# Performance work log

Hardware: AMD Instinct MI355X
Metric: run time of the kernel (lower is better)

The kernel has to match this reference:

```python
import jax, jax.numpy as jnp
import numpy as np

N = 512      # nodes
F_IN = 16    # raw node features; adjacency channels = 2*F_IN = 32
H = 64       # hidden
HF = 64      # hidden_final
C = 10       # num_classes
L = 3        # num_layers
E = 16384    # edges (avg degree 32)
EPS = 1e-5


def setup_inputs() -> dict:
    key = jax.random.key(0)
    ks = iter(jax.random.split(key, 40))
    rn = lambda shape, s=0.05: jax.random.normal(next(ks), shape, jnp.float32) * s
    inp = {
        'x': jax.random.normal(next(ks), (N, F_IN), jnp.float32),
        'edge_index': jax.random.randint(next(ks), (2, E), 0, N),
        # no_prop FeatureExtractor
        'np1_w': rn((HF, 2 * F_IN)), 'np1_b': rn((HF,)),
        'np2_w': rn((HF, 2 * F_IN)), 'np3_w': rn((HF, HF)),
        # first PowerfulLayer (in = 2*F_IN)
        'c0_m1_w': rn((H, 2 * F_IN)), 'c0_m1_b': rn((H,)),
        'c0_m2_w': rn((H, 2 * F_IN)), 'c0_m2_b': rn((H,)),
        'c0_m4_w': rn((H, 2 * F_IN + H)), 'c0_m4_b': rn((H,)),
        # remaining L-1 PowerfulLayers (stacked)
        'cm1_w': rn((L - 1, H, H)), 'cm1_b': rn((L - 1, H)),
        'cm2_w': rn((L - 1, H, H)), 'cm2_b': rn((L - 1, H)),
        'cm4_w': rn((L - 1, H, 2 * H)), 'cm4_b': rn((L - 1, H)),
        # batchnorms (training-mode stats; affine params)
        'bn_g': jnp.ones((L, H), jnp.float32), 'bn_b': jnp.zeros((L, H), jnp.float32),
        # per-layer FeatureExtractors (stacked)
        'fe1_w': rn((L, HF, H)), 'fe1_b': rn((L, HF)),
        'fe2_w': rn((L, HF, H)), 'fe3_w': rn((L, HF, HF)),
        # after_conv and final linear
        'ac_w': rn((HF, HF)), 'ac_b': rn((HF,)),
        'fl_w': rn((C, HF)), 'fl_b': rn((C,)),
    }
    return inp


def _lin(x, w, b=None):
    y = x @ w.T
    return y if b is None else y + b


def _extractor(u, w1, b1, w2, w3):
    # u: [B, N, N, F]; graph_class=True, aggr='add'
    n = u.shape[1]
    trace = jnp.einsum('biif->bf', u)                     # sum of diagonal entries
    out1 = _lin(trace / n, w1, b1)
    s = (u.sum(axis=(1, 2)) - trace) / (n * (n - 1))      # off-diagonal mean-ish
    out = out1 + _lin(s, w2)
    return out + _lin(jax.nn.relu(out), w3)


def _powerful(u, m1w, m1b, m2w, m2b, m4w, m4b):
    # UnitMLP with 1 layer == 1x1 conv == per-position linear (no ReLU)
    o1 = jnp.einsum('bijc,oc->bijo', u, m1w) + m1b        # [B,N,N,H]
    o2 = jnp.einsum('bijc,oc->bijo', u, m2w) + m2b
    mult = jnp.einsum('bikh,bkjh->bijh', o1, o2)          # per-channel NxN matmul
    return _lin(jnp.concatenate([mult, u], axis=-1), m4w, m4b)


def _batchnorm(u, g, b):
    # BatchNorm2d in training mode: stats over (batch, N, N) per channel, biased var
    mean = u.mean(axis=(0, 1, 2))
    var = u.var(axis=(0, 1, 2))
    return (u - mean) * jax.lax.rsqrt(var + EPS) * g + b


def reference(x, edge_index, np1_w, np1_b, np2_w, np3_w,
              c0_m1_w, c0_m1_b, c0_m2_w, c0_m2_b, c0_m4_w, c0_m4_b,
              cm1_w, cm1_b, cm2_w, cm2_b, cm4_w, cm4_b,
              bn_g, bn_b, fe1_w, fe1_b, fe2_w, fe3_w,
              ac_w, ac_b, fl_w, fl_b):
    n = x.shape[0]
    src, dst = edge_index[0], edge_index[1]
    edge_attr = jnp.concatenate([x[src], x[dst]], axis=-1)          # [E, 2F]
    A = jnp.zeros((n, n, edge_attr.shape[-1]), x.dtype).at[src, dst].add(edge_attr)
    u = A[None]                                                      # [1,N,N,2F]

    out = _extractor(u, np1_w, np1_b, np2_w, np3_w)
    nlayers = bn_g.shape[0]
    for l in range(nlayers):
        if l == 0:
            u = _powerful(u, c0_m1_w, c0_m1_b, c0_m2_w, c0_m2_b, c0_m4_w, c0_m4_b)
        else:
            u = _powerful(u, cm1_w[l - 1], cm1_b[l - 1], cm2_w[l - 1], cm2_b[l - 1],
                          cm4_w[l - 1], cm4_b[l - 1])
        u = _batchnorm(u, bn_g[l], bn_b[l])
        out = out + _extractor(u, fe1_w[l], fe1_b[l], fe2_w[l], fe3_w[l])

    out = jax.nn.relu(out) / nlayers
    out = out + jax.nn.relu(_lin(out, ac_w, ac_b))   # layer_after_conv
    # dropout with p=0.0 / eval mode is identity
    out = _lin(out, fl_w, fl_b)
    return jax.nn.log_softmax(out, axis=-1)          # [1, num_classes]
```

## Files before the change

### kernel.cpp

```cpp
#include <hip/hip_runtime.h>
#include <hip/hip_bf16.h>

#define Nn   512
#define NN   262144
#define EDG  16384

typedef unsigned short u16;
typedef unsigned int u32;
typedef short v8s __attribute__((ext_vector_type(8)));
typedef float v4f __attribute__((ext_vector_type(4)));
typedef u16 u16x8 __attribute__((ext_vector_type(8)));

__device__ __forceinline__ float b2f(u16 u) {
    union { unsigned int i; float f; } v; v.i = ((unsigned int)u) << 16; return v.f;
}
__device__ __forceinline__ u16 f2b(float f) {
    union { float f; unsigned int i; } v; v.f = f;
    unsigned int r = (v.i + 0x7FFFu + ((v.i >> 16) & 1u)) >> 16;
    return (u16)r;
}

__global__ void sentinel_kernel(float* __restrict__ out, float val) {
    if (threadIdx.x < 10) out[threadIdx.x] = val;
}

__global__ void cvt_weights(const float* __restrict__ s0, const float* __restrict__ s1,
                            const float* __restrict__ s2, const float* __restrict__ s3,
                            const float* __restrict__ s4, const float* __restrict__ s5,
                            u16* __restrict__ dst) {
    int t = blockIdx.x * 256 + threadIdx.x;
    if (t >= 43008) return;
    float v;
    if      (t < 2048)  v = s0[t];
    else if (t < 4096)  v = s1[t - 2048];
    else if (t < 10240) v = s2[t - 4096];
    else if (t < 18432) v = s3[t - 10240];
    else if (t < 26624) v = s4[t - 18432];
    else                v = s5[t - 26624];
    dst[t] = f2b(v);
}

__global__ void scatter_edges(const float* __restrict__ x, const int* __restrict__ ei,
                              float* __restrict__ A) {
    int t = blockIdx.x * 256 + threadIdx.x;
    if (t >= EDG * 32) return;
    int e = t >> 5, c = t & 31;
    int s = ei[e], d = ei[EDG + e];
    float v = (c < 16) ? x[s * 16 + c] : x[d * 16 + (c - 16)];
    atomicAdd(A + ((size_t)s * Nn + d) * 32 + c, v);
}

__global__ __launch_bounds__(256) void finalize_u0(const float* __restrict__ A,
                                                   u16* __restrict__ u0,
                                                   float* __restrict__ total) {
    __shared__ u16 L[32 * 258];
    __shared__ float red[4][32];
    int t = threadIdx.x;
    int p0 = blockIdx.x * 256;
    const float* Ar = A + (size_t)(p0 + t) * 32;
    float v[32];
#pragma unroll
    for (int c = 0; c < 32; ++c) v[c] = Ar[c];
#pragma unroll
    for (int c = 0; c < 32; ++c) L[c * 258 + t] = f2b(v[c]);
    int wv = t >> 6;
#pragma unroll
    for (int c = 0; c < 32; ++c) {
        float r = v[c];
        for (int off = 32; off > 0; off >>= 1) r += __shfl_down(r, off);
        if ((t & 63) == 0) red[wv][c] = r;
    }
    __syncthreads();
    if (t < 32) atomicAdd(total + t, red[0][t] + red[1][t] + red[2][t] + red[3][t]);
    int off = (t & 31) * 8, rb = t >> 5;
#pragma unroll
    for (int pass = 0; pass < 4; ++pass) {
        int c = pass * 8 + rb;
        u16x8 w = *(const u16x8*)(L + c * 258 + off);
        *(u16x8*)(u0 + (size_t)c * NN + p0 + off) = w;
    }
}

__global__ void trace_raw_cm(const u16* __restrict__ ucm, float* __restrict__ trraw) {
    int c = blockIdx.x, t = threadIdx.x;
    const u16* base = ucm + (size_t)c * NN;
    float s = b2f(base[(size_t)(2 * t) * 513]) + b2f(base[(size_t)(2 * t + 1) * 513]);
    for (int off = 32; off > 0; off >>= 1) s += __shfl_down(s, off);
    __shared__ float r[4];
    if ((t & 63) == 0) r[t >> 6] = s;
    __syncthreads();
    if (t == 0) trraw[c] = r[0] + r[1] + r[2] + r[3];
}

template<int NCH>
__global__ __launch_bounds__(256) void conv12_t(
    const u16* __restrict__ src,
    const float* __restrict__ sc, const float* __restrict__ sh,
    const u16* __restrict__ w1, const float* __restrict__ b1,
    const u16* __restrict__ w2, const float* __restrict__ b2,
    u16* __restrict__ dst1, u16* __restrict__ dst2)
{
    __shared__ u16 LS[8320];
    const int C = NCH * 32;
    const int t = threadIdx.x;
    const int P0 = blockIdx.x * 128;
    const int lane = t & 63, wave = t >> 6;
    const int l15 = lane & 15, quad = lane >> 4;
    const int pw = wave * 32;
    const int sr = t >> 4;
    const int so = (t & 15) * 8;

    u16x8 pf[NCH][2];
#pragma unroll
    for (int kc = 0; kc < NCH; ++kc)
#pragma unroll
        for (int ps = 0; ps < 2; ++ps)
            pf[kc][ps] = *(const u16x8*)(src + (size_t)(kc * 32 + ps * 16 + sr) * NN + P0 + so);

    v4f acc[2][4][2];
#pragma unroll
    for (int s = 0; s < 2; ++s)
#pragma unroll
        for (int mt = 0; mt < 4; ++mt)
#pragma unroll
            for (int nt = 0; nt < 2; ++nt) acc[s][mt][nt] = (v4f){0.f, 0.f, 0.f, 0.f};

    {
        u16* Ln = LS;
#pragma unroll
        for (int ps = 0; ps < 2; ++ps) {
            int c = ps * 16 + sr;
            u16x8 v = pf[0][ps];
            if (sc) {
                float s = sc[c], f = sh[c];
#pragma unroll
                for (int j = 0; j < 8; ++j) v[j] = f2b(b2f(v[j]) * s + f);
            }
            *(u16x8*)(Ln + c * 130 + so) = v;
        }
    }
    __syncthreads();
#pragma unroll
    for (int kc = 0; kc < NCH; ++kc) {
        if (kc + 1 < NCH) {
            u16* Ln = LS + ((kc + 1) & 1) * 4160;
#pragma unroll
            for (int ps = 0; ps < 2; ++ps) {
                int c = ps * 16 + sr;
                int cg = (kc + 1) * 32 + c;
                u16x8 v = pf[kc + 1][ps];
                if (sc) {
                    float s = sc[cg], f = sh[cg];
#pragma unroll
                    for (int j = 0; j < 8; ++j) v[j] = f2b(b2f(v[j]) * s + f);
                }
                *(u16x8*)(Ln + c * 130 + so) = v;
            }
        }
        v8s af1[4], af2[4];
#pragma unroll
        for (int mt = 0; mt < 4; ++mt) {
            af1[mt] = *(const v8s*)(w1 + (mt * 16 + l15) * C + kc * 32 + quad * 8);
            af2[mt] = *(const v8s*)(w2 + (mt * 16 + l15) * C + kc * 32 + quad * 8);
        }
        const u16* Lb = LS + (kc & 1) * 4160;
#pragma unroll
        for (int nt = 0; nt < 2; ++nt) {
            const int p = pw + nt * 16 + l15;
            v8s b;
#pragma unroll
            for (int j = 0; j < 8; ++j) b[j] = (short)Lb[(quad * 8 + j) * 130 + p];
#pragma unroll
            for (int mt = 0; mt < 4; ++mt) {
                acc[0][mt][nt] = __builtin_amdgcn_mfma_f32_16x16x32_bf16(af1[mt], b, acc[0][mt][nt], 0, 0, 0);
                acc[1][mt][nt] = __builtin_amdgcn_mfma_f32_16x16x32_bf16(af2[mt], b, acc[1][mt][nt], 0, 0, 0);
            }
        }
        if (kc + 1 < NCH) __syncthreads();
    }
#pragma unroll
    for (int s = 0; s < 2; ++s) {
        __syncthreads();
        const float* bb = s ? b2 : b1;
#pragma unroll
        for (int mt = 0; mt < 4; ++mt)
#pragma unroll
            for (int r = 0; r < 4; ++r) {
                const int h = mt * 16 + quad * 4 + r;
                const float bv = bb[h];
#pragma unroll
                for (int nt = 0; nt < 2; ++nt)
                    LS[h * 130 + pw + nt * 16 + l15] = f2b(acc[s][mt][nt][r] + bv);
            }
        __syncthreads();
        u16* dd = s ? dst2 : dst1;
#pragma unroll
        for (int ps = 0; ps < 4; ++ps) {
            int h = ps * 16 + sr;
            u16x8 v = *(const u16x8*)(LS + h * 130 + so);
            __builtin_nontemporal_store(v, (u16x8*)(dd + (size_t)h * NN + P0 + so));
        }
    }
}

template<int NCH>
__global__ __launch_bounds__(256) void conv4_t(
    const u16* __restrict__ mult, const u16* __restrict__ u,
    const float* __restrict__ sc, const float* __restrict__ sh,
    const u16* __restrict__ w, const float* __restrict__ bias,
    u16* __restrict__ dst,
    float* __restrict__ psum, float* __restrict__ psq, float* __restrict__ ptr)
{
    __shared__ u16 LS[8320];
    __shared__ float R1[64][4], R2[64][4];
    const int K = NCH * 32;
    const int t = threadIdx.x;
    const int P0 = blockIdx.x * 128;
    const int lane = t & 63, wave = t >> 6;
    const int l15 = lane & 15, quad = lane >> 4;
    const int pw = wave * 32;
    const int sr = t >> 4;
    const int so = (t & 15) * 8;

    u16x8 pf[NCH][2];
#pragma unroll
    for (int kc = 0; kc < NCH; ++kc)
#pragma unroll
        for (int ps = 0; ps < 2; ++ps) {
            int cg = kc * 32 + ps * 16 + sr;
            const u16* gp = (cg < 64) ? (mult + (size_t)cg * NN + P0 + so)
                                      : (u + (size_t)(cg - 64) * NN + P0 + so);
            pf[kc][ps] = *(const u16x8*)gp;
        }

    v4f acc[4][2];
#pragma unroll
    for (int mt = 0; mt < 4; ++mt)
#pragma unroll
        for (int nt = 0; nt < 2; ++nt) acc[mt][nt] = (v4f){0.f, 0.f, 0.f, 0.f};

#pragma unroll
    for (int ps = 0; ps < 2; ++ps)
        *(u16x8*)(LS + (ps * 16 + sr) * 130 + so) = pf[0][ps];
    __syncthreads();
#pragma unroll
    for (int kc = 0; kc < NCH; ++kc) {
        if (kc + 1 < NCH) {
            u16* Ln = LS + ((kc + 1) & 1) * 4160;
#pragma unroll
            for (int ps = 0; ps < 2; ++ps) {
                int c = ps * 16 + sr;
                int cg = (kc + 1) * 32 + c;
                u16x8 v = pf[kc + 1][ps];
                if (cg >= 64 && sc) {
                    float s = sc[cg - 64], f = sh[cg - 64];
#pragma unroll
                    for (int j = 0; j < 8; ++j) v[j] = f2b(b2f(v[j]) * s + f);
                }
                *(u16x8*)(Ln + c * 130 + so) = v;
            }
        }
        v8s af[4];
#pragma unroll
        for (int mt = 0; mt < 4; ++mt)
            af[mt] = *(const v8s*)(w + (mt * 16 + l15) * K + kc * 32 + quad * 8);
        const u16* Lb = LS + (kc & 1) * 4160;
#pragma unroll
        for (int nt = 0; nt < 2; ++nt) {
            const int p = pw + nt * 16 + l15;
            v8s b;
#pragma unroll
            for (int j = 0; j < 8; ++j) b[j] = (short)Lb[(quad * 8 + j) * 130 + p];
#pragma unroll
            for (int mt = 0; mt < 4; ++mt)
                acc[mt][nt] = __builtin_amdgcn_mfma_f32_16x16x32_bf16(af[mt], b, acc[mt][nt], 0, 0, 0);
        }
        if (kc + 1 < NCH) __syncthreads();
    }
    __syncthreads();
#pragma unroll
    for (int mt = 0; mt < 4; ++mt)
#pragma unroll
        for (int r = 0; r < 4; ++r) {
            const int h = mt * 16 + quad * 4 + r;
            const float bv = bias[h];
#pragma unroll
            for (int nt = 0; nt < 2; ++nt)
                LS[h * 130 + pw + nt * 16 + l15] = f2b(acc[mt][nt][r] + bv);
        }
    __syncthreads();
    {
        int c = t >> 2, q = t & 3;
        const u16* row = LS + c * 130 + q * 32;
        float s = 0.f, s2 = 0.f;
#pragma unroll
        for (int i = 0; i < 32; ++i) { float v = b2f(row[i]); s += v; s2 += v * v; }
        R1[c][q] = s; R2[c][q] = s2;
    }
    __syncthreads();
    {
        int i = P0 >> 9, j0 = P0 & 511;
        int blk = blockIdx.x;
        if (t < 64) {
            psum[t * 2048 + blk] = R1[t][0] + R1[t][1] + R1[t][2] + R1[t][3];
            psq[t * 2048 + blk]  = R2[t][0] + R2[t][1] + R2[t][2] + R2[t][3];
            if (j0 <= i && i < j0 + 128) ptr[t * 512 + i] = b2f(LS[t * 130 + (i - j0)]);
        }
    }
#pragma unroll
    for (int ps = 0; ps < 4; ++ps) {
        int h = ps * 16 + sr;
        u16x8 v = *(const u16x8*)(LS + h * 130 + so);
        __builtin_nontemporal_store(v, (u16x8*)(dst + (size_t)h * NN + P0 + so));
    }
}

__global__ __launch_bounds__(512, 2) void bmm_mfma256(const u16* __restrict__ Aall,
                                                      const u16* __restrict__ Ball,
                                                      u16* __restrict__ Call) {
    __shared__ u16 LA[2][16384];
    __shared__ u16 LB[2][16384];

    const int bid = blockIdx.x;
    const int h  = ((bid >> 5) << 3) | (bid & 7);
    const int qq = (bid >> 3) & 3;
    const int ty = qq >> 1, tx = qq & 1;
    const int t = threadIdx.x;
    const int l = t & 63, w = t >> 6;
    const int l15 = l & 15, quad = l >> 4;
    const int wr = w >> 2, wc = w & 3;

    const u16* Ap = Aall + (size_t)h * NN + (size_t)ty * 256 * 512;
    const u16* Bp = Ball + (size_t)h * NN + tx * 256;
    u16* Cp = Call + (size_t)h * NN;

    const int a_m = l >> 3;
    const int a_kg = (l & 7) ^ a_m;
    const u16* ApL = Ap + (size_t)a_m * 512 + a_kg * 8;

    v4f acc[8][4];
#pragma unroll
    for (int mt = 0; mt < 8; ++mt)
#pragma unroll
        for (int nt = 0; nt < 4; ++nt) acc[mt][nt] = (v4f){0.f, 0.f, 0.f, 0.f};

    uint2 eB[4], oB[4];

#define BMM_BLOAD(K0)                                                         \
    _Pragma("unroll")                                                         \
    for (int L = 0; L < 4; ++L) {                                             \
        const int p = w + 8 * L;                                              \
        const u16* s_ = Bp + (size_t)((K0) + 2 * p) * 512 + l * 4;            \
        eB[L] = *(const uint2*)s_;                                            \
        oB[L] = *(const uint2*)(s_ + 512);                                    \
    }

#define BMM_ALOAD(BUF, K0)                                                    \
    _Pragma("unroll")                                                         \
    for (int c = 0; c < 4; ++c) {                                             \
        const int cc = w * 4 + c;                                             \
        __builtin_amdgcn_global_load_lds(                                     \
            (const void*)(ApL + (size_t)cc * 4096 + (K0)),                    \
            (void*)&LA[BUF][cc * 512], 16, 0, 0);                             \
    }

#define BMM_BWRITE(BUF)                                                       \
    {                                                                         \
        char* base_ = (char*)&LB[BUF][0];                                     \
        _Pragma("unroll")                                                     \
        for (int L = 0; L < 4; ++L) {                                         \
            const int p = w + 8 * L;                                          \
            const int gk = p >> 2, wd = p & 3;                                \
            u32 e0 = eB[L].x, e1 = eB[L].y, o0 = oB[L].x, o1 = oB[L].y;       \
            u32 pk0 = (e0 & 0xFFFFu) | (o0 << 16);                            \
            u32 pk1 = (e0 >> 16) | (o0 & 0xFFFF0000u);                        \
            u32 pk2 = (e1 & 0xFFFFu) | (o1 << 16);                            \
            u32 pk3 = (e1 >> 16) | (o1 & 0xFFFF0000u);                        \
            _Pragma("unroll")                                                 \
            for (int q = 0; q < 4; ++q) {                                     \
                const int j = l * 4 + q;                                      \
                const int g = gk ^ (j & 7) ^ ((j >> 3) & 7);                  \
                u32 v_ = (q == 0) ? pk0 : (q == 1) ? pk1 : (q == 2) ? pk2 : pk3; \
                *(u32*)(base_ + j * 128 + (g << 4) + wd * 4) = v_;            \
            }                                                                 \
        }                                                                     \
    }

#define BMM_COMPUTE(BUF)                                                      \
    _Pragma("unroll")                                                         \
    for (int kk = 0; kk < 2; ++kk) {                                          \
        v8s af_[8], bf_[4];                                                   \
        const char* baseA_ = (const char*)&LA[BUF][0];                        \
        const char* baseB_ = (const char*)&LB[BUF][0];                        \
        _Pragma("unroll")                                                     \
        for (int mt = 0; mt < 8; ++mt) {                                      \
            const int m = wr * 128 + mt * 16 + l15;                           \
            const int g = (kk * 4 + quad) ^ (m & 7);                          \
            af_[mt] = *(const v8s*)(baseA_ + m * 128 + (g << 4));             \
        }                                                                     \
        _Pragma("unroll")                                                     \
        for (int nt = 0; nt < 4; ++nt) {                                      \
            const int j = wc * 64 + nt * 16 + l15;                            \
            const int g = (kk * 4 + quad) ^ (j & 7) ^ ((j >> 3) & 7);         \
            bf_[nt] = *(const v8s*)(baseB_ + j * 128 + (g << 4));             \
        }                                                                     \
        _Pragma("unroll")                                                     \
        for (int mt = 0; mt < 8; ++mt)                                        \
            _Pragma("unroll")                                                 \
            for (int nt = 0; nt < 4; ++nt)                                    \
                acc[mt][nt] = __builtin_amdgcn_mfma_f32_16x16x32_bf16(        \
                    af_[mt], bf_[nt], acc[mt][nt], 0, 0, 0);                  \
    }

    BMM_BLOAD(0)
    BMM_ALOAD(0, 0)
    BMM_BWRITE(0)
    __syncthreads();

#pragma unroll 2
    for (int ts = 0; ts < 8; ++ts) {
        const int cur = ts & 1;
        if (ts < 7) {
            BMM_BLOAD((ts + 1) * 64)
            BMM_ALOAD(cur ^ 1, (ts + 1) * 64)
        }
        BMM_COMPUTE(cur)
        if (ts < 7) {
            BMM_BWRITE(cur ^ 1)
            __syncthreads();
        }
    }

#pragma unroll
    for (int mt = 0; mt < 8; ++mt)
#pragma unroll
        for (int r = 0; r < 4; ++r) {
            const int i = ty * 256 + wr * 128 + mt * 16 + quad * 4 + r;
#pragma unroll
            for (int nt = 0; nt < 4; ++nt) {
                const int j = tx * 256 + wc * 64 + nt * 16 + l15;
                Cp[(size_t)i * 512 + j] = f2b(acc[mt][nt][r]);
            }
        }
#undef BMM_BLOAD
#undef BMM_ALOAD
#undef BMM_BWRITE
#undef BMM_COMPUTE
}

__global__ __launch_bounds__(256) void bn_finalize(
    const float* __restrict__ psum, const float* __restrict__ psq,
    const float* __restrict__ ptr,
    const float* __restrict__ g, const float* __restrict__ b,
    float* __restrict__ scale, float* __restrict__ shift,
    float* __restrict__ ttl) {
    int c = blockIdx.x, t = threadIdx.x;
    float s = 0.f, q = 0.f, tr = 0.f;
    for (int k = t; k < 2048; k += 256) { s += psum[c * 2048 + k]; q += psq[c * 2048 + k]; }
    for (int k = t; k < 512; k += 256) tr += ptr[c * 512 + k];
    for (int off = 32; off > 0; off >>= 1) {
        s += __shfl_down(s, off); q += __shfl_down(q, off); tr += __shfl_down(tr, off);
    }
    __shared__ float r1[4], r2[4], r3[4];
    if ((t & 63) == 0) { r1[t >> 6] = s; r2[t >> 6] = q; r3[t >> 6] = tr; }
    __syncthreads();
    if (t == 0) {
        s = r1[0] + r1[1] + r1[2] + r1[3];
        q = r2[0] + r2[1] + r2[2] + r2[3];
        tr = r3[0] + r3[1] + r3[2] + r3[3];
        float mean = s * (1.f / 262144.f);
        float var = q * (1.f / 262144.f) - mean * mean;
        float sc = g[c] * rsqrtf(fmaxf(var, 0.f) + 1e-5f);
        float sh = b[c] - mean * sc;
        scale[c] = sc;
        shift[c] = sh;
        ttl[64 + c] = sc * s + 262144.f * sh;
        ttl[c]      = sc * tr + 512.f * sh;
    }
}

__global__ __launch_bounds__(256) void extractor_par(
    const float* __restrict__ tt,
    const float* __restrict__ np1w, const float* __restrict__ np1b,
    const float* __restrict__ np2w, const float* __restrict__ np3w,
    const float* __restrict__ fe1w, const float* __restrict__ fe1b,
    const float* __restrict__ fe2w, const float* __restrict__ fe3w,
    float* __restrict__ oacc_part) {
    __shared__ float red[64][4];
    __shared__ float xo[64];
    const int li = blockIdx.x;
    const int t = threadIdx.x;
    const int h = t >> 2, q = t & 3;
    const int C = (li == 0) ? 32 : 64;
    const float* w1 = (li == 0) ? np1w : fe1w + (li - 1) * 4096;
    const float* b1 = (li == 0) ? np1b : fe1b + (li - 1) * 64;
    const float* w2 = (li == 0) ? np2w : fe2w + (li - 1) * 4096;
    const float* w3 = (li == 0) ? np3w : fe3w + (li - 1) * 4096;
    const float* tr = tt + li * 128;
    const float* to = tr + 64;
    const int cpq = C >> 2;
    float p = 0.f;
    for (int i = 0; i < cpq; ++i) {
        int c = q * cpq + i;
        p += (tr[c] * (1.f / 512.f)) * w1[h * C + c]
           + ((to[c] - tr[c]) * (1.f / (512.f * 511.f))) * w2[h * C + c];
    }
    red[h][q] = p;
    __syncthreads();
    if (q == 0) xo[h] = b1[h] + red[h][0] + red[h][1] + red[h][2] + red[h][3];
    __syncthreads();
    float o = xo[h];
    float p3 = 0.f;
    for (int i = 0; i < 16; ++i) {
        int f = q * 16 + i;
        p3 += fmaxf(xo[f], 0.f) * w3[h * 64 + f];
    }
    __syncthreads();
    red[h][q] = p3;
    __syncthreads();
    if (q == 0) oacc_part[li * 64 + h] = o + red[h][0] + red[h][1] + red[h][2] + red[h][3];
}

__global__ __launch_bounds__(256) void head_par(
    const float* __restrict__ oacc_part,
    const float* __restrict__ acw, const float* __restrict__ acb,
    const float* __restrict__ flw, const float* __restrict__ flb,
    float* __restrict__ out) {
    __shared__ float x[64], x2[64], red[64][4], l[10];
    const int t = threadIdx.x;
    const int h = t >> 2, q = t & 3;
    if (q == 0) {
        float oa = oacc_part[h] + oacc_part[64 + h] + oacc_part[128 + h] + oacc_part[192 + h];
        x[h] = fmaxf(oa, 0.f) * (1.f / 3.f);
    }
    __syncthreads();
    float p = 0.f;
    for (int i = 0; i < 16; ++i) { int f = q * 16 + i; p += x[f] * acw[h * 64 + f]; }
    red[h][q] = p;
    __syncthreads();
    if (q == 0) {
        float y = acb[h] + red[h][0] + red[h][1] + red[h][2] + red[h][3];
        x2[h] = x[h] + fmaxf(y, 0.f);
    }
    __syncthreads();
    if (t < 40) {
        int hh = t >> 2, qq = t & 3;
        float p2 = 0.f;
        for (int i = 0; i < 16; ++i) { int f = qq * 16 + i; p2 += x2[f] * flw[hh * 64 + f]; }
        red[hh][qq] = p2;
    }
    __syncthreads();
    if (t < 10) l[t] = flb[t] + red[t][0] + red[t][1] + red[t][2] + red[t][3];
    __syncthreads();
    if (t == 0) {
        float m = l[0];
        for (int i = 1; i < 10; ++i) m = fmaxf(m, l[i]);
        float se = 0.f;
        for (int i = 0; i < 10; ++i) se += expf(l[i] - m);
        float ls = m + logf(se);
        for (int i = 0; i < 10; ++i) out[i] = l[i] - ls;
    }
}

extern "C" void kernel_launch(void* const* d_in, const int* in_sizes, int n_in,
                              void* d_out, int out_size, void* d_ws, size_t ws_size,
                              hipStream_t stream) {
    float* out = (float*)d_out;

    static const int exp_sizes[28] = {
        8192, 32768,
        2048, 64, 2048, 4096,
        2048, 64, 2048, 64, 6144, 64,
        8192, 128, 8192, 128, 16384, 128,
        192, 192,
        12288, 192, 12288, 12288,
        4096, 64, 640, 10
    };
    bool ok = (n_in == 28);
    if (ok) for (int i = 0; i < 28; ++i) if (in_sizes[i] != exp_sizes[i]) ok = false;
    if (!ok) { sentinel_kernel<<<1, 64, 0, stream>>>(out, -5.0f); return; }

    const size_t RSZ = (size_t)NN * 64 * 2;
    const size_t BIG_OFF = 8192 + 90112;
    if (ws_size < BIG_OFF + 4 * RSZ) {
        sentinel_kernel<<<1, 64, 0, stream>>>(out, -7.0f);
        return;
    }

    const float* x     = (const float*)d_in[0];
    const int*   ei    = (const int*)d_in[1];
    const float* np1w  = (const float*)d_in[2];
    const float* np1b  = (const float*)d_in[3];
    const float* np2w  = (const float*)d_in[4];
    const float* np3w  = (const float*)d_in[5];
    const float* c0m1b = (const float*)d_in[7];
    const float* c0m2b = (const float*)d_in[9];
    const float* c0m4b = (const float*)d_in[11];
    const float* cm1b  = (const float*)d_in[13];
    const float* cm2b  = (const float*)d_in[15];
    const float* cm4b  = (const float*)d_in[17];
    const float* bng   = (const float*)d_in[18];
    const float* bnb   = (const float*)d_in[19];
    const float* fe1w  = (const float*)d_in[20];
    const float* fe1b  = (const float*)d_in[21];
    const float* fe2w  = (const float*)d_in[22];
    const float* fe3w  = (const float*)d_in[23];
    const float* acw   = (const float*)d_in[24];
    const float* acb   = (const float*)d_in[25];
    const float* flw   = (const float*)d_in[26];
    const float* flb   = (const float*)d_in[27];

    char* ws = (char*)d_ws;
    float* small = (float*)ws;
    float* tt    = small;
    float* scl   = small + 512;
    float* shf   = small + 576;
    float* oaccp = small + 640;

    u16* arena = (u16*)(ws + 8192);

    char* big = ws + BIG_OFF;
    u16* S0 = (u16*)(big + 0 * RSZ);
    u16* S1 = (u16*)(big + 1 * RSZ);
    u16* S2 = (u16*)(big + 2 * RSZ);
    u16* S3 = (u16*)(big + 3 * RSZ);
    float* Abuf = (float*)S2;

    float* psum = (float*)S2;
    float* psq  = psum + 64 * 2048;
    float* ptr  = psq + 64 * 2048;

    hipMemsetAsync(small, 0, 4096, stream);
    hipMemsetAsync(Abuf, 0, (size_t)NN * 32 * 4, stream);

    cvt_weights<<<168, 256, 0, stream>>>((const float*)d_in[6], (const float*)d_in[8],
                                         (const float*)d_in[10], (const float*)d_in[12],
                                         (const float*)d_in[14], (const float*)d_in[16], arena);
    scatter_edges<<<2048, 256, 0, stream>>>(x, ei, Abuf);
    finalize_u0<<<1024, 256, 0, stream>>>(Abuf, S0, tt + 64);
    trace_raw_cm<<<32, 256, 0, stream>>>(S0, tt);

    u16* U[3]  = { S0, S1, S0 };
    u16* O1[3] = { S1, S0, S1 };
    u16* R[3]  = { S1, S0, S1 };

    const float *aff_s = nullptr, *aff_h = nullptr;

    for (int l = 0; l < 3; ++l) {
        int Cin = (l == 0) ? 32 : 64;
        const u16 *w1b, *w2b, *w4b;
        const float *b1, *b2, *b4;
        if (l == 0) {
            w1b = arena;            b1 = c0m1b;
            w2b = arena + 2048;     b2 = c0m2b;
            w4b = arena + 4096;     b4 = c0m4b;
        } else {
            int m = l - 1;
            w1b = arena + 10240 + m * 4096;  b1 = cm1b + m * 64;
            w2b = arena + 18432 + m * 4096;  b2 = cm2b + m * 64;
            w4b = arena + 26624 + m * 8192;  b4 = cm4b + m * 64;
        }
        if (Cin == 32)
            conv12_t<1><<<2048, 256, 0, stream>>>(U[l], aff_s, aff_h, w1b, b1, w2b, b2, O1[l], S2);
        else
            conv12_t<2><<<2048, 256, 0, stream>>>(U[l], aff_s, aff_h, w1b, b1, w2b, b2, O1[l], S2);
        bmm_mfma256<<<256, 512, 0, stream>>>(O1[l], S2, S3);
        if (Cin == 32)
            conv4_t<3><<<2048, 256, 0, stream>>>(S3, U[l], aff_s, aff_h, w4b, b4, R[l], psum, psq, ptr);
        else
            conv4_t<4><<<2048, 256, 0, stream>>>(S3, U[l], aff_s, aff_h, w4b, b4, R[l], psum, psq, ptr);
        bn_finalize<<<64, 256, 0, stream>>>(psum, psq, ptr, bng + l * 64, bnb + l * 64,
                                            scl, shf, tt + (l + 1) * 128);
        aff_s = scl; aff_h = shf;
    }
    extractor_par<<<4, 256, 0, stream>>>(tt, np1w, np1b, np2w, np3w,
                                         fe1w, fe1b, fe2w, fe3w, oaccp);
    head_par<<<1, 256, 0, stream>>>(oaccp, acw, acb, flw, flb, out);
}
```

Measured before the change: 467.1 us.

## Restructure conv12 into persistent 512-thread blocks with swizzled position-major LDS tiles

Replaces the conv12 kernel with a version where each 512-thread block handles 512 positions over four 128-position tiles. Weights and biases are loaded into registers once per block, global loads for the next tile are double-buffered against MFMA compute, and the LDS tile is stored position-major with an XOR swizzle so B fragments can be read as 16-byte vectors instead of eight scalar reads. The aim is to cut redundant weight loads, LDS bank conflicts and per-block overhead. In exchange, outputs are now written as scattered 2-byte nontemporal stores instead of coalesced 16-byte stores, and register pressure rises.

```diff
diff --git a/kernel.cpp b/kernel.cpp
--- a/kernel.cpp
+++ b/kernel.cpp
@@ -18,6 +18,11 @@
     union { float f; unsigned int i; } v; v.f = f;
     unsigned int r = (v.i + 0x7FFFu + ((v.i >> 16) & 1u)) >> 16;
     return (u16)r;
+}
+__device__ __forceinline__ u32 aff2(u32 x, float s, float h) {
+    float lo = b2f((u16)(x & 0xFFFFu)) * s + h;
+    float hi = b2f((u16)(x >> 16)) * s + h;
+    return (u32)f2b(lo) | ((u32)f2b(hi) << 16);
 }
 
 __global__ void sentinel_kernel(float* __restrict__ out, float val) {
@@ -92,115 +97,153 @@
     if (t == 0) trraw[c] = r[0] + r[1] + r[2] + r[3];
 }
 
-template<int NCH>
-__global__ __launch_bounds__(256) void conv12_t(
+template<int CIN>
+__global__ __launch_bounds__(512, 4) void conv12_s(
     const u16* __restrict__ src,
     const float* __restrict__ sc, const float* __restrict__ sh,
     const u16* __restrict__ w1, const float* __restrict__ b1,
     const u16* __restrict__ w2, const float* __restrict__ b2,
     u16* __restrict__ dst1, u16* __restrict__ dst2)
 {
-    __shared__ u16 LS[8320];
-    const int C = NCH * 32;
+    constexpr int G    = CIN / 8;
+    constexpr int LOGG = (CIN == 64) ? 3 : 2;
+    constexpr int ROWB = CIN * 2;
+    constexpr int KC   = CIN / 32;
+    constexpr int PASSES = CIN / 32;
+
+    __shared__ char LB[2][128 * ROWB];
+
     const int t = threadIdx.x;
-    const int P0 = blockIdx.x * 128;
-    const int lane = t & 63, wave = t >> 6;
+    const int lane = t & 63, w = t >> 6;
     const int l15 = lane & 15, quad = lane >> 4;
-    const int pw = wave * 32;
-    const int sr = t >> 4;
-    const int so = (t & 15) * 8;
-
-    u16x8 pf[NCH][2];
-#pragma unroll
-    for (int kc = 0; kc < NCH; ++kc)
-#pragma unroll
-        for (int ps = 0; ps < 2; ++ps)
-            pf[kc][ps] = *(const u16x8*)(src + (size_t)(kc * 32 + ps * 16 + sr) * NN + P0 + so);
-
-    v4f acc[2][4][2];
-#pragma unroll
-    for (int s = 0; s < 2; ++s)
-#pragma unroll
-        for (int mt = 0; mt < 4; ++mt)
-#pragma unroll
-            for (int nt = 0; nt < 2; ++nt) acc[s][mt][nt] = (v4f){0.f, 0.f, 0.f, 0.f};
-
-    {
-        u16* Ln = LS;
-#pragma unroll
-        for (int ps = 0; ps < 2; ++ps) {
-            int c = ps * 16 + sr;
-            u16x8 v = pf[0][ps];
-            if (sc) {
-                float s = sc[c], f = sh[c];
-#pragma unroll
-                for (int j = 0; j < 8; ++j) v[j] = f2b(b2f(v[j]) * s + f);
+    const int wr = w >> 1;
+    const int wn = w & 1;
+    const size_t Pblk = (size_t)blockIdx.x * 512;
+
+    const int cpair = (CIN == 64) ? (t >> 4) : (t >> 5);
+    const int pg    = (CIN == 64) ? (t & 15) : (t & 31);
+    const int g0    = cpair >> 2;
+    const int word  = cpair & 3;
+    const u16* srcA = src + (size_t)(2 * cpair) * NN;
+    float s0 = 1.f, h0 = 0.f, s1 = 1.f, h1 = 0.f;
+    const bool aff = (sc != nullptr);
+    if (aff) { s0 = sc[2 * cpair]; h0 = sh[2 * cpair]; s1 = sc[2 * cpair + 1]; h1 = sh[2 * cpair + 1]; }
+
+    v8s af[2][KC];
+#pragma unroll
+    for (int mt = 0; mt < 2; ++mt) {
+        const int row = wr * 32 + mt * 16 + l15;
+        const u16* Wm = (row < 64) ? (w1 + row * CIN) : (w2 + (row - 64) * CIN);
+#pragma unroll
+        for (int kc = 0; kc < KC; ++kc)
+            af[mt][kc] = *(const v8s*)(Wm + kc * 32 + quad * 8);
+    }
+    float bias[2][4];
+#pragma unroll
+    for (int mt = 0; mt < 2; ++mt)
+#pragma unroll
+        for (int r = 0; r < 4; ++r) {
+            const int row = wr * 32 + mt * 16 + quad * 4 + r;
+            bias[mt][r] = (row < 64) ? b1[row] : b2[row - 64];
+        }
+
+    v4f acc[2][4];
+#pragma unroll
+    for (int mt = 0; mt < 2; ++mt)
+#pragma unroll
+        for (int nt = 0; nt < 4; ++nt) acc[mt][nt] = (v4f){0.f, 0.f, 0.f, 0.f};
+
+    uint2 ea[PASSES], eb[PASSES];
+
+#define C12_LOAD(T)                                                           \
+    _Pragma("unroll")                                                         \
+    for (int pp = 0; pp < PASSES; ++pp) {                                     \
+        const int p0_ = (pg + ((CIN == 64) ? 16 : 0) * pp) * 4;               \
+        const u16* sp_ = srcA + Pblk + (size_t)(T) * 128 + p0_;               \
+        ea[pp] = *(const uint2*)sp_;                                          \
+        eb[pp] = *(const uint2*)(sp_ + NN);                                   \
+    }
+
+#define C12_WRITE(BUF)                                                        \
+    {                                                                         \
+        char* Lb_ = LB[BUF];                                                  \
+        _Pragma("unroll")                                                     \
+        for (int pp = 0; pp < PASSES; ++pp) {                                 \
+            const int p0_ = (pg + ((CIN == 64) ? 16 : 0) * pp) * 4;           \
+            u32 A0 = ea[pp].x, A1 = ea[pp].y, B0 = eb[pp].x, B1 = eb[pp].y;   \
+            if (aff) {                                                        \
+                A0 = aff2(A0, s0, h0); A1 = aff2(A1, s0, h0);                 \
+                B0 = aff2(B0, s1, h1); B1 = aff2(B1, s1, h1);                 \
+            }                                                                 \
+            u32 pk0 = (A0 & 0xFFFFu) | (B0 << 16);                            \
+            u32 pk1 = (A0 >> 16) | (B0 & 0xFFFF0000u);                        \
+            u32 pk2 = (A1 & 0xFFFFu) | (B1 << 16);                            \
+            u32 pk3 = (A1 >> 16) | (B1 & 0xFFFF0000u);                        \
+            _Pragma("unroll")                                                 \
+            for (int w4 = 0; w4 < 4; ++w4) {                                  \
+                const int p_ = p0_ + w4;                                      \
+                const int g_ = g0 ^ (p_ & (G - 1)) ^ ((p_ >> LOGG) & (G - 1));\
+                u32 v_ = (w4 == 0) ? pk0 : (w4 == 1) ? pk1 : (w4 == 2) ? pk2 : pk3; \
+                *(u32*)(Lb_ + p_ * ROWB + g_ * 16 + word * 4) = v_;           \
+            }                                                                 \
+        }                                                                     \
+    }
+
+#define C12_COMPUTE(BUF)                                                      \
+    _Pragma("unroll")                                                         \
+    for (int kc = 0; kc < KC; ++kc) {                                         \
+        v8s bf_[4];                                                           \
+        const char* Lb_ = LB[BUF];                                            \
+        _Pragma("unroll")                                                     \
+        for (int nt = 0; nt < 4; ++nt) {                                      \
+            const int p_ = wn * 64 + nt * 16 + l15;                           \
+            const int lg_ = kc * 4 + quad;                                    \
+            const int g_ = lg_ ^ (p_ & (G - 1)) ^ ((p_ >> LOGG) & (G - 1));   \
+            bf_[nt] = *(const v8s*)(Lb_ + p_ * ROWB + g_ * 16);               \
+        }                                                                     \
+        _Pragma("unroll")                                                     \
+        for (int mt = 0; mt < 2; ++mt)                                        \
+            _Pragma("unroll")                                                 \
+            for (int nt = 0; nt < 4; ++nt)                                    \
+                acc[mt][nt] = __builtin_amdgcn_mfma_f32_16x16x32_bf16(        \
+                    af[mt][kc], bf_[nt], acc[mt][nt], 0, 0, 0);               \
+    }
+
+    C12_LOAD(0)
+    C12_WRITE(0)
+    __syncthreads();
+
+#pragma unroll
+    for (int T = 0; T < 4; ++T) {
+        const int cur = T & 1;
+        if (T < 3) C12_LOAD(T + 1)
+        C12_COMPUTE(cur)
+#pragma unroll
+        for (int mt = 0; mt < 2; ++mt)
+#pragma unroll
+            for (int r = 0; r < 4; ++r) {
+                const int row = wr * 32 + mt * 16 + quad * 4 + r;
+                u16* dp = ((row < 64) ? (dst1 + (size_t)row * NN)
+                                      : (dst2 + (size_t)(row - 64) * NN))
+                          + Pblk + (size_t)T * 128 + wn * 64 + l15;
+#pragma unroll
+                for (int nt = 0; nt < 4; ++nt) {
+                    u16 v = f2b(acc[mt][nt][r] + bias[mt][r]);
+                    __builtin_nontemporal_store(v, dp + nt * 16);
+                }
             }
-            *(u16x8*)(Ln + c * 130 + so) = v;
-        }
-    }
-    __syncthreads();
-#pragma unroll
-    for (int kc = 0; kc < NCH; ++kc) {
-        if (kc + 1 < NCH) {
-            u16* Ln = LS + ((kc + 1) & 1) * 4160;
-#pragma unroll
-            for (int ps = 0; ps < 2; ++ps) {
-                int c = ps * 16 + sr;
-                int cg = (kc + 1) * 32 + c;
-                u16x8 v = pf[kc + 1][ps];
-                if (sc) {
-                    float s = sc[cg], f = sh[cg];
-#pragma unroll
-                    for (int j = 0; j < 8; ++j) v[j] = f2b(b2f(v[j]) * s + f);
-                }
-                *(u16x8*)(Ln + c * 130 + so) = v;
-            }
-        }
-        v8s af1[4], af2[4];
-#pragma unroll
-        for (int mt = 0; mt < 4; ++mt) {
-            af1[mt] = *(const v8s*)(w1 + (mt * 16 + l15) * C + kc * 32 + quad * 8);
-            af2[mt] = *(const v8s*)(w2 + (mt * 16 + l15) * C + kc * 32 + quad * 8);
-        }
-        const u16* Lb = LS + (kc & 1) * 4160;
-#pragma unroll
-        for (int nt = 0; nt < 2; ++nt) {
-            const int p = pw + nt * 16 + l15;
-            v8s b;
-#pragma unroll
-            for (int j = 0; j < 8; ++j) b[j] = (short)Lb[(quad * 8 + j) * 130 + p];
-#pragma unroll
-            for (int mt = 0; mt < 4; ++mt) {
-                acc[0][mt][nt] = __builtin_amdgcn_mfma_f32_16x16x32_bf16(af1[mt], b, acc[0][mt][nt], 0, 0, 0);
-                acc[1][mt][nt] = __builtin_amdgcn_mfma_f32_16x16x32_bf16(af2[mt], b, acc[1][mt][nt], 0, 0, 0);
-            }
-        }
-        if (kc + 1 < NCH) __syncthreads();
-    }
-#pragma unroll
-    for (int s = 0; s < 2; ++s) {
-        __syncthreads();
-        const float* bb = s ? b2 : b1;
-#pragma unroll
-        for (int mt = 0; mt < 4; ++mt)
-#pragma unroll
-            for (int r = 0; r < 4; ++r) {
-                const int h = mt * 16 + quad * 4 + r;
-                const float bv = bb[h];
-#pragma unroll
-                for (int nt = 0; nt < 2; ++nt)
-                    LS[h * 130 + pw + nt * 16 + l15] = f2b(acc[s][mt][nt][r] + bv);
-            }
-        __syncthreads();
-        u16* dd = s ? dst2 : dst1;
-#pragma unroll
-        for (int ps = 0; ps < 4; ++ps) {
-            int h = ps * 16 + sr;
-            u16x8 v = *(const u16x8*)(LS + h * 130 + so);
-            __builtin_nontemporal_store(v, (u16x8*)(dd + (size_t)h * NN + P0 + so));
-        }
-    }
+#pragma unroll
+        for (int mt = 0; mt < 2; ++mt)
+#pragma unroll
+            for (int nt = 0; nt < 4; ++nt) acc[mt][nt] = (v4f){0.f,0.f,0.f,0.f};
+        if (T < 3) {
+            C12_WRITE(cur ^ 1)
+            __syncthreads();
+        }
+    }
+#undef C12_LOAD
+#undef C12_WRITE
+#undef C12_COMPUTE
 }
 
 template<int NCH>
@@ -661,9 +704,9 @@
             w4b = arena + 26624 + m * 8192;  b4 = cm4b + m * 64;
         }
         if (Cin == 32)
-            conv12_t<1><<<2048, 256, 0, stream>>>(U[l], aff_s, aff_h, w1b, b1, w2b, b2, O1[l], S2);
+            conv12_s<32><<<512, 512, 0, stream>>>(U[l], aff_s, aff_h, w1b, b1, w2b, b2, O1[l], S2);
         else
-            conv12_t<2><<<2048, 256, 0, stream>>>(U[l], aff_s, aff_h, w1b, b1, w2b, b2, O1[l], S2);
+            conv12_s<64><<<512, 512, 0, stream>>>(U[l], aff_s, aff_h, w1b, b1, w2b, b2, O1[l], S2);
         bmm_mfma256<<<256, 512, 0, stream>>>(O1[l], S2, S3);
         if (Cin == 32)
             conv4_t<3><<<2048, 256, 0, stream>>>(S3, U[l], aff_s, aff_h, w4b, b4, R[l], psum, psq, ptr);
```

Measured after the change: 462.3 us. No clear change (-1.0%).
